# Kernel tuning notes

Hardware: AMD Instinct MI355X
Metric: run time of the kernel (lower is better)

The kernel has to match this reference:

```python
import jax, jax.numpy as jnp
import numpy as np


def _softsplat(tenIn, tenFlow):
    """Bilinear forward splatting: scatter tenIn to flow-displaced locations.
    tenIn: [N,C,H,W], tenFlow: [N,2,H,W] -> out [N,C,H,W]."""
    N, C, H, W = tenIn.shape
    dt = tenIn.dtype
    gx = jnp.arange(W, dtype=dt)[None, None, :]   # [1,1,W]
    gy = jnp.arange(H, dtype=dt)[None, :, None]   # [1,H,1]
    fx = gx + tenFlow[:, 0]                       # [N,H,W] target x
    fy = gy + tenFlow[:, 1]                       # [N,H,W] target y
    finite = jnp.isfinite(fx) & jnp.isfinite(fy)
    x0f = jnp.floor(fx)
    y0f = jnp.floor(fy)
    ix0 = x0f.astype(jnp.int32)
    iy0 = y0f.astype(jnp.int32)
    # bilinear corner weights (NW, NE, SW, SE) exactly as in the CUDA kernel
    wx1 = fx - x0f            # weight toward east
    wx0 = (x0f + 1.0) - fx    # weight toward west
    wy1 = fy - y0f            # weight toward south
    wy0 = (y0f + 1.0) - fy    # weight toward north
    corners = [
        (ix0,     iy0,     wx0 * wy0),  # NW
        (ix0 + 1, iy0,     wx1 * wy0),  # NE
        (ix0,     iy0 + 1, wx0 * wy1),  # SW
        (ix0 + 1, iy0 + 1, wx1 * wy1),  # SE
    ]
    HW = H * W
    tenIn_flat = tenIn.reshape(N, C, HW)

    def scatter_corner(ix, iy, w):
        valid = finite & (ix >= 0) & (ix < W) & (iy >= 0) & (iy < H)
        idx = jnp.where(valid, iy * W + ix, 0).reshape(N, HW)       # [N,HW]
        wv = jnp.where(valid, w, jnp.zeros_like(w)).reshape(N, 1, HW)
        vals = (tenIn_flat * wv).transpose(0, 2, 1)                 # [N,HW,C]
        seg = jax.vmap(lambda v, i: jax.ops.segment_sum(v, i, num_segments=HW))(vals, idx)
        return seg                                                   # [N,HW,C]

    out = scatter_corner(*corners[0])
    for c in corners[1:]:
        out = out + scatter_corner(*c)
    return out.transpose(0, 2, 1).reshape(N, C, H, W)


def softsplat_softmax(tenIn, tenFlow, tenMetric):
    # strMode == 'softmax': splat [tenIn * exp(metric), exp(metric)], then normalize
    w = jnp.exp(tenMetric)                          # [N,1,H,W]
    packed = jnp.concatenate([tenIn * w, w], axis=1)
    out = _softsplat(packed, tenFlow)
    norm = out[:, -1:]
    norm = jnp.where(norm == 0.0, jnp.ones_like(norm), norm)
    return out[:, :-1] / norm


def setup_inputs() -> dict:
    key = jax.random.key(0)
    k1, k2, k3 = jax.random.split(key, 3)
    N, C, H, W = 8, 64, 288, 512
    tenIn = jax.random.normal(k1, (N, C, H, W), dtype=jnp.float32)
    tenFlow = jax.random.normal(k2, (N, 2, H, W), dtype=jnp.float32)
    tenMetric = jax.random.normal(k3, (N, 1, H, W), dtype=jnp.float32)
    return {"tenIn": tenIn, "tenFlow": tenFlow, "tenMetric": tenMetric}


def reference(tenIn, tenFlow, tenMetric):
    return softsplat_softmax(tenIn, tenFlow, tenMetric)
```

## Files before the change

kernel.cpp:

```cpp
#include <hip/hip_runtime.h>
#include <hip/hip_fp16.h>
#include <math.h>

constexpr int N  = 8;
constexpr int C  = 64;
constexpr int H  = 288;
constexpr int W  = 512;
constexpr int HW = H * W;
constexpr int NPIX = N * HW;

constexpr int TW = 64, TH = 32, R = 8;
constexpr int PW = TW + 2 * R;
constexpr int PH = TH + 2 * R;
constexpr int PS = PW * PH;
constexpr int TGX = W / TW;
constexpr int TGY = H / TH;
constexpr int TILES = N * TGX * TGY;
constexpr int NOUT = TH * TW;
constexpr int K = 12;
constexpr int CCHB = 4;
constexpr int NCHUNK = C / CCHB;
constexpr int NSPLIT = 2;
constexpr int CPB = NCHUNK / NSPLIT;
constexpr int OVFCAP = 256;
constexpr int ESCCAP = 512;
constexpr int NTC = 512;
constexpr int NTG = 1024;
constexpr int GGRID = TILES * NSPLIT;

constexpr size_t WS_DEN  = 0;
constexpr size_t WS_META = WS_DEN  + (size_t)N * HW;
constexpr size_t WS_CNT  = WS_META + (size_t)TILES * NOUT * K;
constexpr size_t WS_OVFC = WS_CNT  + (size_t)TILES * NOUT;
constexpr size_t WS_OVFE = WS_OVFC + TILES;
constexpr size_t WS_ESCC = WS_OVFE + (size_t)TILES * OVFCAP * 2;
constexpr size_t WS_ESCE = WS_ESCC + TILES;

__device__ __forceinline__ int swz(int si) { return si ^ ((si >> 4) & 15); }

__device__ __forceinline__ unsigned packh2(float a, float b) {
    __half2 h = __floats2half2_rn(a, b);
    return *reinterpret_cast<unsigned*>(&h);
}
__device__ __forceinline__ float2 unpackh2(unsigned u) {
    __half2 h = *reinterpret_cast<__half2*>(&u);
    return __half22float2(h);
}

__global__ __launch_bounds__(NTC) void claim_kernel(
    const float* __restrict__ flow, const float* __restrict__ metric,
    unsigned* __restrict__ meta,
    unsigned* __restrict__ ovfc, unsigned* __restrict__ ovfe,
    float* __restrict__ den)
{
    __shared__ unsigned cnt[NOUT];
    for (int i = threadIdx.x; i < NOUT; i += NTC) cnt[i] = 0;
    __syncthreads();

    const int t  = blockIdx.x;
    const int n  = t / (TGX * TGY);
    const int r  = t % (TGX * TGY);
    const int Y0 = (r / TGX) * TH;
    const int X0 = (r % TGX) * TW;

    const float* fxp = flow + ((size_t)n * 2) * HW;
    const float* fyp = fxp + HW;
    const float* mp  = metric + (size_t)n * HW;
    unsigned* mt = meta + (size_t)t * K * NOUT;

    for (int si = threadIdx.x; si < PS; si += NTC) {
        int ys = Y0 - R + si / PW;
        int xs = X0 - R + si % PW;
        if ((unsigned)ys >= (unsigned)H || (unsigned)xs >= (unsigned)W) continue;
        int p = ys * W + xs;
        float fx = fxp[p] + (float)xs;
        float fy = fyp[p] + (float)ys;
        if (!(isfinite(fx) && isfinite(fy))) continue;
        float x0f = floorf(fx), y0f = floorf(fy);
        int tx = (int)x0f - X0;
        int ty = (int)y0f - Y0;
        float wx1 = fx - x0f, wx0 = x0f + 1.0f - fx;
        float wy1 = fy - y0f, wy0 = y0f + 1.0f - fy;
        float wm  = __expf(mp[p]);

        #define CLAIM(TYv, TXv, Wv)                                           \
            if ((unsigned)(TYv) < (unsigned)TH &&                             \
                (unsigned)(TXv) < (unsigned)TW) {                             \
                float w_ = (Wv) * wm;                                         \
                int   o_ = (TYv) * TW + (TXv);                                \
                unsigned slot = atomicAdd(&cnt[o_], 1u);                      \
                if (slot < (unsigned)K) {                                     \
                    mt[(size_t)slot * NOUT + o_] =                            \
                        ((unsigned)__half_as_ushort(__float2half(w_)) << 16)  \
                        | (unsigned)si;                                       \
                } else {                                                      \
                    unsigned p2 = atomicAdd(&ovfc[t], 1u);                    \
                    if (p2 < (unsigned)OVFCAP) {                              \
                        unsigned* e = ovfe + ((size_t)t * OVFCAP + p2) * 2;   \
                        e[0] = ((unsigned)o_ << 16) | (unsigned)si;           \
                        e[1] = __float_as_uint(w_);                           \
                    }                                                         \
                }                                                             \
            }
        CLAIM(ty,     tx,     wx0 * wy0)
        CLAIM(ty,     tx + 1, wx1 * wy0)
        CLAIM(ty + 1, tx,     wx0 * wy1)
        CLAIM(ty + 1, tx + 1, wx1 * wy1)
        #undef CLAIM
    }
    __syncthreads();

    const unsigned on = min(ovfc[t], (unsigned)OVFCAP);
    const unsigned* oe = ovfe + (size_t)t * OVFCAP * 2;
    for (int o = threadIdx.x; o < NOUT; o += NTC) {
        unsigned cn = min(cnt[o], (unsigned)K);
        float d = 0.0f;
        for (unsigned s = 0; s < cn; ++s)
            d += __half2float(__ushort_as_half(
                     (unsigned short)(mt[(size_t)s * NOUT + o] >> 16)));
        for (unsigned s = cn; s < (unsigned)K; ++s)
            mt[(size_t)s * NOUT + o] = 0u;
        for (unsigned i = 0; i < on; ++i)
            if ((oe[2 * i] >> 16) == (unsigned)o)
                d += __uint_as_float(oe[2 * i + 1]);
        den[(size_t)n * HW + (Y0 + o / TW) * W + X0 + o % TW] = d;
    }
}

__global__ __launch_bounds__(256) void escape_kernel(
    const float* __restrict__ flow, const float* __restrict__ metric,
    float* __restrict__ den, unsigned* __restrict__ escc,
    unsigned* __restrict__ esce)
{
    int pix = blockIdx.x * 256 + threadIdx.x;
    if (pix >= NPIX) return;
    int n  = pix / HW;
    int p  = pix - n * HW;
    int xs = p & (W - 1);
    int ys = p >> 9;

    float fx = flow[((size_t)n * 2    ) * HW + p] + (float)xs;
    float fy = flow[((size_t)n * 2 + 1) * HW + p] + (float)ys;
    if (!(isfinite(fx) && isfinite(fy))) return;
    float x0f = floorf(fx), y0f = floorf(fy);
    int ix0 = (int)x0f, iy0 = (int)y0f;
    float wx1 = fx - x0f, wx0 = x0f + 1.0f - fx;
    float wy1 = fy - y0f, wy0 = y0f + 1.0f - fy;

    int   cx[4] = { ix0, ix0 + 1, ix0,     ix0 + 1 };
    int   cy[4] = { iy0, iy0,     iy0 + 1, iy0 + 1 };
    float cw[4] = { wx0 * wy0, wx1 * wy0, wx0 * wy1, wx1 * wy1 };

    bool esc[4]; bool any = false;
    #pragma unroll
    for (int k = 0; k < 4; ++k) {
        esc[k] = false;
        if ((unsigned)cx[k] < (unsigned)W && (unsigned)cy[k] < (unsigned)H) {
            int tX0 = cx[k] & ~(TW - 1);
            int tY0 = cy[k] & ~(TH - 1);
            bool inpad = (xs >= tX0 - R) && (xs < tX0 + TW + R) &&
                         (ys >= tY0 - R) && (ys < tY0 + TH + R);
            if (!inpad) { esc[k] = true; any = true; }
        }
    }
    if (!any) return;

    float wm = __expf(metric[(size_t)n * HW + p]);
    #pragma unroll
    for (int k = 0; k < 4; ++k) {
        if (!esc[k]) continue;
        int tX0 = cx[k] & ~(TW - 1);
        int tY0 = cy[k] & ~(TH - 1);
        int tt  = n * (TGX * TGY) + (tY0 >> 5) * TGX + (tX0 >> 6);
        float w_ = cw[k] * wm;
        atomicAdd(den + (size_t)n * HW + cy[k] * W + cx[k], w_);
        unsigned pos = atomicAdd(&escc[tt], 1u);
        if (pos < (unsigned)ESCCAP) {
            unsigned* e = esce + ((size_t)tt * ESCCAP + pos) * 3;
            e[0] = (unsigned)((cy[k] - tY0) * TW + (cx[k] - tX0));
            e[1] = (unsigned)p;
            e[2] = __float_as_uint(w_);
        }
    }
}

__global__ __launch_bounds__(NTG, 4) void gather_kernel(
    const float* __restrict__ in, const unsigned* __restrict__ meta,
    const unsigned* __restrict__ ovfc,
    const unsigned* __restrict__ ovfe, const unsigned* __restrict__ escc,
    const unsigned* __restrict__ esce, const float* __restrict__ den,
    float* __restrict__ out)
{
    __shared__ uint2 val[PS];

    const int b0 = blockIdx.x;
    const int b  = (b0 & 7) * (GGRID / 8) + (b0 >> 3);
    const int t     = b >> 1;
    const int split = b & 1;
    const int n  = t / (TGX * TGY);
    const int r  = t % (TGX * TGY);
    const int Y0 = (r / TGX) * TH;
    const int X0 = (r % TGX) * TW;

    const unsigned on = min(ovfc[t], (unsigned)OVFCAP);
    const unsigned en = min(escc[t], (unsigned)ESCCAP);
    const unsigned* oe = ovfe + (size_t)t * OVFCAP * 2;
    const unsigned* ee = esce + (size_t)t * ESCCAP * 3;
    const unsigned* mt = meta + (size_t)t * K * NOUT;

    float inv[2];
    int   opix[2];
    #pragma unroll
    for (int k = 0; k < 2; ++k) {
        int o = threadIdx.x + k * NTG;
        opix[k] = (Y0 + o / TW) * W + X0 + o % TW;
        float d = den[(size_t)n * HW + opix[k]];
        inv[k] = (d == 0.0f) ? 1.0f : 1.0f / d;
    }

    for (int cc = 0; cc < CPB; ++cc) {
        const int cb = split * CPB + cc;
        const float* inb = in + ((size_t)n * C + cb * CCHB) * HW;
        __syncthreads();
        if (threadIdx.x < PS / 4) {
            int si0 = threadIdx.x * 4;
            int row = si0 / PW;
            int ys  = Y0 - R + row;
            int xs0 = X0 - R + (si0 - row * PW);
            bool ok = (unsigned)ys < (unsigned)H && (unsigned)xs0 < (unsigned)W;
            const float* pp = inb + ys * W + xs0;
            float4 g0 = {0,0,0,0}, g1 = g0, g2 = g0, g3 = g0;
            if (ok) {
                g0 = *reinterpret_cast<const float4*>(pp);
                g1 = *reinterpret_cast<const float4*>(pp + HW);
                g2 = *reinterpret_cast<const float4*>(pp + 2 * HW);
                g3 = *reinterpret_cast<const float4*>(pp + 3 * HW);
            }
            int sw = (si0 >> 4) & 15;
            val[(si0    ) ^ sw] = make_uint2(packh2(g0.x, g1.x), packh2(g2.x, g3.x));
            val[(si0 + 1) ^ sw] = make_uint2(packh2(g0.y, g1.y), packh2(g2.y, g3.y));
            val[(si0 + 2) ^ sw] = make_uint2(packh2(g0.z, g1.z), packh2(g2.z, g3.z));
            val[(si0 + 3) ^ sw] = make_uint2(packh2(g0.w, g1.w), packh2(g2.w, g3.w));
        }
        __syncthreads();

        #pragma unroll
        for (int k = 0; k < 2; ++k) {
            const int o = threadIdx.x + k * NTG;
            const unsigned* mo = mt + o;
            unsigned mloc[K];
            #pragma unroll
            for (int s = 0; s < K; ++s) mloc[s] = mo[(size_t)s * NOUT];

            float a0 = 0.0f, a1 = 0.0f, a2 = 0.0f, a3 = 0.0f;
            #pragma unroll
            for (int s = 0; s < K; ++s) {
                unsigned m_ = mloc[s];
                float w  = __half2float(__ushort_as_half((unsigned short)(m_ >> 16)));
                int   si = (int)(m_ & 0xffffu);
                uint2 v = val[swz(si)];
                float2 f0 = unpackh2(v.x), f1 = unpackh2(v.y);
                a0 += w * f0.x;  a1 += w * f0.y;
                a2 += w * f1.x;  a3 += w * f1.y;
            }
            for (unsigned i = 0; i < on; ++i) {
                unsigned e0 = oe[2 * i];
                if ((e0 >> 16) == (unsigned)o) {
                    float w  = __uint_as_float(oe[2 * i + 1]);
                    uint2 v = val[swz((int)(e0 & 0xffffu))];
                    float2 f0 = unpackh2(v.x), f1 = unpackh2(v.y);
                    a0 += w * f0.x;  a1 += w * f0.y;
                    a2 += w * f1.x;  a3 += w * f1.y;
                }
            }
            for (unsigned i = 0; i < en; ++i) {
                if (ee[3 * i] == (unsigned)o) {
                    float w  = __uint_as_float(ee[3 * i + 2]);
                    int   ps = (int)ee[3 * i + 1];
                    a0 += w * inb[ps];
                    a1 += w * inb[ps + HW];
                    a2 += w * inb[ps + 2 * HW];
                    a3 += w * inb[ps + 3 * HW];
                }
            }
            size_t ob = ((size_t)n * C + cb * CCHB) * HW + opix[k];
            out[ob]          = a0 * inv[k];
            out[ob + HW]     = a1 * inv[k];
            out[ob + 2 * HW] = a2 * inv[k];
            out[ob + 3 * HW] = a3 * inv[k];
        }
    }
}

extern "C" void kernel_launch(void* const* d_in, const int* in_sizes, int n_in,
                              void* d_out, int out_size, void* d_ws, size_t ws_size,
                              hipStream_t stream)
{
    const float* tenIn     = (const float*)d_in[0];
    const float* tenFlow   = (const float*)d_in[1];
    const float* tenMetric = (const float*)d_in[2];
    float* out = (float*)d_out;

    unsigned* ws  = (unsigned*)d_ws;
    float*    den = (float*)(ws + WS_DEN);
    unsigned* meta = ws + WS_META;
    unsigned* ovfc = ws + WS_OVFC;
    unsigned* ovfe = ws + WS_OVFE;
    unsigned* escc = ws + WS_ESCC;
    unsigned* esce = ws + WS_ESCE;

    hipMemsetAsync(ovfc, 0, TILES * sizeof(unsigned), stream);
    hipMemsetAsync(escc, 0, TILES * sizeof(unsigned), stream);

    claim_kernel<<<TILES, NTC, 0, stream>>>(tenFlow, tenMetric,
                                            meta, ovfc, ovfe, den);
    escape_kernel<<<(NPIX + 255) / 256, 256, 0, stream>>>(tenFlow, tenMetric,
                                                          den, escc, esce);
    gather_kernel<<<GGRID, NTG, 0, stream>>>(tenIn, meta, ovfc,
                                             ovfe, escc, esce, den, out);
}
```

Measured before the change: 271.9 us.

## Double-buffer gather staging and store per-output meta slots contiguously

```diff
diff --git a/kernel.cpp b/kernel.cpp
--- a/kernel.cpp
+++ b/kernel.cpp
@@ -66,7 +66,7 @@
     const float* fxp = flow + ((size_t)n * 2) * HW;
     const float* fyp = fxp + HW;
     const float* mp  = metric + (size_t)n * HW;
-    unsigned* mt = meta + (size_t)t * K * NOUT;
+    unsigned* mt = meta + (size_t)t * NOUT * K;
 
     for (int si = threadIdx.x; si < PS; si += NTC) {
         int ys = Y0 - R + si / PW;
@@ -82,6 +82,7 @@
         float wx1 = fx - x0f, wx0 = x0f + 1.0f - fx;
         float wy1 = fy - y0f, wy0 = y0f + 1.0f - fy;
         float wm  = __expf(mp[p]);
+        int sis = swz(si);
 
         #define CLAIM(TYv, TXv, Wv)                                           \
             if ((unsigned)(TYv) < (unsigned)TH &&                             \
@@ -90,14 +91,14 @@
                 int   o_ = (TYv) * TW + (TXv);                                \
                 unsigned slot = atomicAdd(&cnt[o_], 1u);                      \
                 if (slot < (unsigned)K) {                                     \
-                    mt[(size_t)slot * NOUT + o_] =                            \
+                    mt[(size_t)o_ * K + slot] =                               \
                         ((unsigned)__half_as_ushort(__float2half(w_)) << 16)  \
-                        | (unsigned)si;                                       \
+                        | (unsigned)sis;                                      \
                 } else {                                                      \
                     unsigned p2 = atomicAdd(&ovfc[t], 1u);                    \
                     if (p2 < (unsigned)OVFCAP) {                              \
                         unsigned* e = ovfe + ((size_t)t * OVFCAP + p2) * 2;   \
-                        e[0] = ((unsigned)o_ << 16) | (unsigned)si;           \
+                        e[0] = ((unsigned)o_ << 16) | (unsigned)sis;          \
                         e[1] = __float_as_uint(w_);                           \
                     }                                                         \
                 }                                                             \
@@ -117,9 +118,9 @@
         float d = 0.0f;
         for (unsigned s = 0; s < cn; ++s)
             d += __half2float(__ushort_as_half(
-                     (unsigned short)(mt[(size_t)s * NOUT + o] >> 16)));
+                     (unsigned short)(mt[(size_t)o * K + s] >> 16)));
         for (unsigned s = cn; s < (unsigned)K; ++s)
-            mt[(size_t)s * NOUT + o] = 0u;
+            mt[(size_t)o * K + s] = 0u;
         for (unsigned i = 0; i < on; ++i)
             if ((oe[2 * i] >> 16) == (unsigned)o)
                 d += __uint_as_float(oe[2 * i + 1]);
@@ -191,7 +192,7 @@
     const unsigned* __restrict__ esce, const float* __restrict__ den,
     float* __restrict__ out)
 {
-    __shared__ uint2 val[PS];
+    __shared__ uint2 val[2][PS];
 
     const int b0 = blockIdx.x;
     const int b  = (b0 & 7) * (GGRID / 8) + (b0 >> 3);
@@ -206,7 +207,7 @@
     const unsigned en = min(escc[t], (unsigned)ESCCAP);
     const unsigned* oe = ovfe + (size_t)t * OVFCAP * 2;
     const unsigned* ee = esce + (size_t)t * ESCCAP * 3;
-    const unsigned* mt = meta + (size_t)t * K * NOUT;
+    const unsigned* mt = meta + (size_t)t * NOUT * K;
 
     float inv[2];
     int   opix[2];
@@ -218,47 +219,67 @@
         inv[k] = (d == 0.0f) ? 1.0f : 1.0f / d;
     }
 
+    const bool stager = threadIdx.x < PS / 4;
+    int si0 = 0, sw = 0, soff = 0;
+    bool ok = false;
+    if (stager) {
+        si0 = threadIdx.x * 4;
+        int row = si0 / PW;
+        int ys  = Y0 - R + row;
+        int xs0 = X0 - R + (si0 - row * PW);
+        ok  = (unsigned)ys < (unsigned)H && (unsigned)xs0 < (unsigned)W;
+        sw  = (si0 >> 4) & 15;
+        soff = ys * W + xs0;
+    }
+    const float* inb0 = in + ((size_t)n * C + split * CPB * CCHB) * HW;
+
+    float4 g0 = {0,0,0,0}, g1 = g0, g2 = g0, g3 = g0;
+    if (stager && ok) {
+        const float* pp = inb0 + soff;
+        g0 = *reinterpret_cast<const float4*>(pp);
+        g1 = *reinterpret_cast<const float4*>(pp + HW);
+        g2 = *reinterpret_cast<const float4*>(pp + 2 * HW);
+        g3 = *reinterpret_cast<const float4*>(pp + 3 * HW);
+    }
+    if (stager) {
+        val[0][(si0    ) ^ sw] = make_uint2(packh2(g0.x, g1.x), packh2(g2.x, g3.x));
+        val[0][(si0 + 1) ^ sw] = make_uint2(packh2(g0.y, g1.y), packh2(g2.y, g3.y));
+        val[0][(si0 + 2) ^ sw] = make_uint2(packh2(g0.z, g1.z), packh2(g2.z, g3.z));
+        val[0][(si0 + 3) ^ sw] = make_uint2(packh2(g0.w, g1.w), packh2(g2.w, g3.w));
+    }
+
+    int cur = 0;
     for (int cc = 0; cc < CPB; ++cc) {
-        const int cb = split * CPB + cc;
-        const float* inb = in + ((size_t)n * C + cb * CCHB) * HW;
         __syncthreads();
-        if (threadIdx.x < PS / 4) {
-            int si0 = threadIdx.x * 4;
-            int row = si0 / PW;
-            int ys  = Y0 - R + row;
-            int xs0 = X0 - R + (si0 - row * PW);
-            bool ok = (unsigned)ys < (unsigned)H && (unsigned)xs0 < (unsigned)W;
-            const float* pp = inb + ys * W + xs0;
-            float4 g0 = {0,0,0,0}, g1 = g0, g2 = g0, g3 = g0;
+        const float* inb = inb0 + (size_t)cc * CCHB * HW;
+
+        if (cc + 1 < CPB && stager) {
+            g0 = make_float4(0,0,0,0); g1 = g0; g2 = g0; g3 = g0;
             if (ok) {
-                g0 = *reinterpret_cast<const float4*>(pp);
-                g1 = *reinterpret_cast<const float4*>(pp + HW);
-                g2 = *reinterpret_cast<const float4*>(pp + 2 * HW);
-                g3 = *reinterpret_cast<const float4*>(pp + 3 * HW);
-            }
-            int sw = (si0 >> 4) & 15;
-            val[(si0    ) ^ sw] = make_uint2(packh2(g0.x, g1.x), packh2(g2.x, g3.x));
-            val[(si0 + 1) ^ sw] = make_uint2(packh2(g0.y, g1.y), packh2(g2.y, g3.y));
-            val[(si0 + 2) ^ sw] = make_uint2(packh2(g0.z, g1.z), packh2(g2.z, g3.z));
-            val[(si0 + 3) ^ sw] = make_uint2(packh2(g0.w, g1.w), packh2(g2.w, g3.w));
-        }
-        __syncthreads();
-
+                const float* pn = inb + (size_t)CCHB * HW + soff;
+                g0 = *reinterpret_cast<const float4*>(pn);
+                g1 = *reinterpret_cast<const float4*>(pn + HW);
+                g2 = *reinterpret_cast<const float4*>(pn + 2 * HW);
+                g3 = *reinterpret_cast<const float4*>(pn + 3 * HW);
+            }
+        }
+
+        const uint2* vb = val[cur];
         #pragma unroll
         for (int k = 0; k < 2; ++k) {
             const int o = threadIdx.x + k * NTG;
-            const unsigned* mo = mt + o;
-            unsigned mloc[K];
-            #pragma unroll
-            for (int s = 0; s < K; ++s) mloc[s] = mo[(size_t)s * NOUT];
+            const uint4* mo4 = reinterpret_cast<const uint4*>(mt + (size_t)o * K);
+            uint4 qa = mo4[0], qb = mo4[1], qc = mo4[2];
+            unsigned mloc[K] = { qa.x, qa.y, qa.z, qa.w,
+                                 qb.x, qb.y, qb.z, qb.w,
+                                 qc.x, qc.y, qc.z, qc.w };
 
             float a0 = 0.0f, a1 = 0.0f, a2 = 0.0f, a3 = 0.0f;
             #pragma unroll
             for (int s = 0; s < K; ++s) {
                 unsigned m_ = mloc[s];
                 float w  = __half2float(__ushort_as_half((unsigned short)(m_ >> 16)));
-                int   si = (int)(m_ & 0xffffu);
-                uint2 v = val[swz(si)];
+                uint2 v = vb[m_ & 0xffffu];
                 float2 f0 = unpackh2(v.x), f1 = unpackh2(v.y);
                 a0 += w * f0.x;  a1 += w * f0.y;
                 a2 += w * f1.x;  a3 += w * f1.y;
@@ -267,7 +288,7 @@
                 unsigned e0 = oe[2 * i];
                 if ((e0 >> 16) == (unsigned)o) {
                     float w  = __uint_as_float(oe[2 * i + 1]);
-                    uint2 v = val[swz((int)(e0 & 0xffffu))];
+                    uint2 v = vb[e0 & 0xffffu];
                     float2 f0 = unpackh2(v.x), f1 = unpackh2(v.y);
                     a0 += w * f0.x;  a1 += w * f0.y;
                     a2 += w * f1.x;  a3 += w * f1.y;
@@ -283,12 +304,21 @@
                     a3 += w * inb[ps + 3 * HW];
                 }
             }
-            size_t ob = ((size_t)n * C + cb * CCHB) * HW + opix[k];
+            size_t ob = ((size_t)n * C + (split * CPB + cc) * CCHB) * HW + opix[k];
             out[ob]          = a0 * inv[k];
             out[ob + HW]     = a1 * inv[k];
             out[ob + 2 * HW] = a2 * inv[k];
             out[ob + 3 * HW] = a3 * inv[k];
         }
+
+        if (cc + 1 < CPB && stager) {
+            uint2* vn = val[cur ^ 1];
+            vn[(si0    ) ^ sw] = make_uint2(packh2(g0.x, g1.x), packh2(g2.x, g3.x));
+            vn[(si0 + 1) ^ sw] = make_uint2(packh2(g0.y, g1.y), packh2(g2.y, g3.y));
+            vn[(si0 + 2) ^ sw] = make_uint2(packh2(g0.z, g1.z), packh2(g2.z, g3.z));
+            vn[(si0 + 3) ^ sw] = make_uint2(packh2(g0.w, g1.w), packh2(g2.w, g3.w));
+        }
+        cur ^= 1;
     }
 }
 
```

After: 269.7 us. About the same (-0.8%).
